# Kernel tuning notes

Measured on AMD Instinct MI355X. Metric: run time of the kernel, lower is better.

The kernel has to match this reference:

```python
import jax, jax.numpy as jnp
import numpy as np
from jax import lax

# ---- static config (from init_kwargs / input_specs) ----
B, NB, C, F = 16, 8192, 3, 64   # batches, points-per-batch, coord dim, feat dim
RATIO, K = 0.125, 16
M = int(RATIO * NB)


def setup_inputs() -> dict:
    key = jax.random.key(0)
    kx, kp = jax.random.split(key)
    x = jax.random.normal(kx, (B * NB, F), dtype=jnp.float32)
    pos = jax.random.normal(kp, (B * NB, C), dtype=jnp.float32)
    batch = (jnp.arange(B * NB, dtype=jnp.int32) // NB).astype(jnp.int32)
    return {"x": x, "pos": pos, "batch": batch}


def _fps_single(pos_b):
    """Sequential farthest point sampling on (NB, C), deterministic start at 0.
    Returns (M,) int32 indices into pos_b."""
    n = pos_b.shape[0]

    def step(carry, _):
        min_d2, last = carry
        d2 = jnp.sum((pos_b - pos_b[last]) ** 2, axis=-1)   # (NB,)
        min_d2 = jnp.minimum(min_d2, d2)
        nxt = jnp.argmax(min_d2).astype(jnp.int32)
        return (min_d2, nxt), last

    init = (jnp.full((n,), jnp.finfo(pos_b.dtype).max, dtype=pos_b.dtype),
            jnp.int32(0))
    _, idx = lax.scan(step, init, None, length=M)
    return idx  # (M,)


def reference(x, pos, batch):
    # batch ids are block-constant (batch[i] = i // NB), so per-batch views are
    # simple reshapes -- same semantics as torch_cluster's batched fps/knn.
    pos_b = pos.reshape(B, NB, C)

    # --- farthest point sampling per batch ---
    fps_idx = jax.vmap(_fps_single)(pos_b)                            # (B, M)
    centroids = jnp.take_along_axis(pos_b, fps_idx[..., None], axis=1)  # (B, M, C)

    # --- k-NN: squared distances centroids -> all points of same batch ---
    d2 = (jnp.sum(centroids ** 2, axis=-1)[..., None]
          - 2.0 * jnp.einsum('bmc,bnc->bmn', centroids, pos_b)
          + jnp.sum(pos_b ** 2, axis=-1)[:, None, :])                 # (B, M, NB)
    _, nn_idx = lax.top_k(-d2, K)                                     # (B, M, K)

    # gather neighbor coordinates (== pos[groups_idx[1]])
    groups = jax.vmap(lambda p, i: p[i])(pos_b, nn_idx.reshape(B, M * K))  # (B, M*K, C)

    return centroids.reshape(B * M, C), groups.reshape(B * M * K, C)
```

## Files before the change

kernel.cpp:

```cpp
#include <hip/hip_runtime.h>
#include <float.h>
#include <math.h>

#define B_   16
#define NB_  8192
#define M_   1024
#define K_   16


typedef float v2f __attribute__((ext_vector_type(2)));

#define FPS_T 256
#define PPT   32
#define NPAIR (PPT/2)
#define NWAVE (FPS_T/64)

__global__ __launch_bounds__(FPS_T, 1) void fps_kernel(const float* __restrict__ pos,
                                                       float* __restrict__ cent)
{
    #pragma clang fp contract(off)
    const int b = blockIdx.x;
    const int t = threadIdx.x;
    const float* pb = pos + (size_t)b * NB_ * 3;
    float* cb = cent + (size_t)b * M_ * 3;

    __shared__ float4 spts[NB_];
    __shared__ unsigned long long wkey[2][NWAVE];

    for (int p = t; p < NB_; p += FPS_T) {
        const float* s = pb + (size_t)p * 3;
        spts[p] = make_float4(s[0], s[1], s[2], 0.0f);
    }

    v2f px2[NPAIR], py2[NPAIR], pz2[NPAIR], md2[NPAIR];
    #pragma unroll
    for (int jj = 0; jj < NPAIR; ++jj) {
        const float* s0 = pb + (size_t)(t*PPT + 2*jj) * 3;
        px2[jj] = (v2f){s0[0], s0[3]};
        py2[jj] = (v2f){s0[1], s0[4]};
        pz2[jj] = (v2f){s0[2], s0[5]};
        md2[jj] = (v2f){FLT_MAX, FLT_MAX};
    }
    __syncthreads();

    float lx = pb[0], ly = pb[1], lz = pb[2];
    float c0x=0,c0y=0,c0z=0,c1x=0,c1y=0,c1z=0,c2x=0,c2y=0,c2z=0,c3x=0,c3y=0,c3z=0;

    for (int m = 0; m < M_; ++m) {
        if (t == (m >> 2)) {
            const int sl = m & 3;
            if      (sl == 0) { c0x=lx; c0y=ly; c0z=lz; }
            else if (sl == 1) { c1x=lx; c1y=ly; c1z=lz; }
            else if (sl == 2) { c2x=lx; c2y=ly; c2z=lz; }
            else              { c3x=lx; c3y=ly; c3z=lz; }
        }
        if (m == M_ - 1) break;

        const v2f lxv = {lx,lx}, lyv = {ly,ly}, lzv = {lz,lz};
        v2f bmax2 = {-1.0f, -1.0f};
        #pragma unroll
        for (int jj = 0; jj < NPAIR; ++jj) {
            v2f dx = px2[jj] - lxv;
            v2f dy = py2[jj] - lyv;
            v2f dz = pz2[jj] - lzv;
            v2f d2 = (dx*dx + dy*dy) + dz*dz;
            v2f mj = __builtin_elementwise_min(md2[jj], d2);
            md2[jj] = mj;
            bmax2 = __builtin_elementwise_max(bmax2, mj);
        }
        float bm = fmaxf(bmax2.x, bmax2.y);

        float v = bm;
        {
            int vi;
            vi = __builtin_amdgcn_update_dpp(__float_as_int(v), __float_as_int(v), 0xB1,  0xF, 0xF, false);
            v = fmaxf(v, __int_as_float(vi));
            vi = __builtin_amdgcn_update_dpp(__float_as_int(v), __float_as_int(v), 0x4E,  0xF, 0xF, false);
            v = fmaxf(v, __int_as_float(vi));
            vi = __builtin_amdgcn_update_dpp(__float_as_int(v), __float_as_int(v), 0x141, 0xF, 0xF, false);
            v = fmaxf(v, __int_as_float(vi));
            vi = __builtin_amdgcn_update_dpp(__float_as_int(v), __float_as_int(v), 0x140, 0xF, 0xF, false);
            v = fmaxf(v, __int_as_float(vi));
            vi = __builtin_amdgcn_update_dpp(__float_as_int(v), __float_as_int(v), 0x142, 0xF, 0xF, false);
            v = fmaxf(v, __int_as_float(vi));
            vi = __builtin_amdgcn_update_dpp(__float_as_int(v), __float_as_int(v), 0x143, 0xF, 0xF, false);
            v = fmaxf(v, __int_as_float(vi));
        }
        const float wv = __int_as_float(__builtin_amdgcn_readlane(__float_as_int(v), 63));

        int jp = -1;
        #pragma unroll
        for (int jj = NPAIR - 1; jj >= 0; --jj) {
            if (md2[jj].y == wv) jp = 2*jj + 1;
            if (md2[jj].x == wv) jp = 2*jj;
        }
        const unsigned long long mk = __ballot(jp >= 0);
        const int wl = (int)__ffsll(mk) - 1;
        const int gi = __builtin_amdgcn_readlane(t*PPT + jp, wl);

        const int par = m & 1;
        if ((t & 63) == 0)
            wkey[par][t >> 6] = ((unsigned long long)__float_as_uint(wv) << 32) |
                                (unsigned int)(~gi);
        __syncthreads();

        unsigned long long kk = wkey[par][0];
        #pragma unroll
        for (int w = 1; w < NWAVE; ++w) {
            const unsigned long long e = wkey[par][w];
            kk = (e > kk) ? e : kk;
        }
        const int best = (int)(~(unsigned int)kk);

        const float4 c = spts[best];
        lx = c.x; ly = c.y; lz = c.z;
    }

    {
        float4* o = (float4*)(cb + (size_t)t * 12);
        o[0] = make_float4(c0x, c0y, c0z, c1x);
        o[1] = make_float4(c1y, c1z, c2x, c2y);
        o[2] = make_float4(c2z, c3x, c3y, c3z);
    }
}

#define KNN_T   256
#define CHUNK   1024
#define GRP     8
#define BCAP    16
#define BSTRIDE 17

__device__ __forceinline__ void topk_insert(float d2, int pi, float val[16], int idx[16])
{
    int r = 0;
    #pragma unroll
    for (int j = 0; j < 16; ++j) r += (val[j] <= d2) ? 1 : 0;
    #pragma unroll
    for (int j = 15; j >= 1; --j) {
        bool sh = (j > r);
        val[j] = sh ? val[j-1] : val[j];
        idx[j] = sh ? idx[j-1] : idx[j];
    }
    #pragma unroll
    for (int j = 0; j < 16; ++j) {
        bool pl = (j == r);
        val[j] = pl ? d2 : val[j];
        idx[j] = pl ? pi : idx[j];
    }
}

__global__ __launch_bounds__(KNN_T, 2) void knn_kernel(const float* __restrict__ pos,
    const float* __restrict__ cent, float* __restrict__ groups,
    unsigned long long* __restrict__ partials, int nsplit)
{
    #pragma clang fp contract(off)
    __shared__ float4 spts[CHUNK];
    __shared__ unsigned long long sbuf[KNN_T * BSTRIDE];

    const int wg = blockIdx.x;
    const int t  = threadIdx.x;
    const int per_b = 4 * nsplit;
    const int b  = wg / per_b;
    const int r  = wg % per_b;
    const int cg = r / nsplit;
    const int sp = r % nsplit;
    const int span  = NB_ / nsplit;
    const int pbase = sp * span;
    const int nchunks = span / CHUNK;

    const float* pb = pos + (size_t)b * NB_ * 3;
    const int mg = b * M_ + cg * KNN_T + t;
    const float cx = cent[(size_t)mg*3+0];
    const float cy = cent[(size_t)mg*3+1];
    const float cz = cent[(size_t)mg*3+2];
    const float cn2 = (cx*cx + cy*cy) + cz*cz;

    float val[16]; int idx[16];
    #pragma unroll
    for (int j = 0; j < 16; ++j) { val[j] = FLT_MAX; idx[j] = 0; }
    float tau = FLT_MAX;
    int cnt = 0;
    unsigned long long* mybuf = sbuf + t * BSTRIDE;

    for (int c = 0; c < nchunks; ++c) {
        const int ps = pbase + c * CHUNK;
        __syncthreads();
        for (int p = t; p < CHUNK; p += KNN_T) {
            const float* s = pb + (size_t)(ps + p) * 3;
            float x = s[0], y = s[1], z = s[2];
            float pn2 = (x*x + y*y) + z*z;
            spts[p] = make_float4(x, y, z, pn2);
        }
        __syncthreads();

        for (int p0 = 0; p0 < CHUNK; p0 += GRP) {
            if (__any(cnt > BCAP - GRP)) {
                int n = cnt; cnt = 0;
                for (int i = 0; i < n; ++i) {
                    unsigned long long e = mybuf[i];
                    float d = __uint_as_float((unsigned int)(e >> 32));
                    int pi  = (int)(e & 0xFFFFFFFFu);
                    if (d < val[15]) topk_insert(d, pi, val, idx);
                }
                tau = val[15];
            }
            float4 q[GRP];
            #pragma unroll
            for (int i = 0; i < GRP; ++i) q[i] = spts[p0 + i];
            float d2v[GRP];
            #pragma unroll
            for (int i = 0; i < GRP; ++i) {
                float dot = __builtin_fmaf(cz, q[i].z,
                            __builtin_fmaf(cy, q[i].y, cx * q[i].x));
                d2v[i] = (cn2 - 2.0f*dot) + q[i].w;
            }
            #pragma unroll
            for (int i = 0; i < GRP; ++i) {
                if (d2v[i] < tau) {
                    mybuf[cnt] = ((unsigned long long)__float_as_uint(d2v[i]) << 32) |
                                 (unsigned int)(ps + p0 + i);
                    ++cnt;
                }
            }
        }
    }
    {
        int n = cnt;
        for (int i = 0; i < n; ++i) {
            unsigned long long e = mybuf[i];
            float d = __uint_as_float((unsigned int)(e >> 32));
            int pi  = (int)(e & 0xFFFFFFFFu);
            if (d < val[15]) topk_insert(d, pi, val, idx);
        }
    }

    if (nsplit > 1) {
        unsigned long long* o = partials + ((size_t)mg * nsplit + sp) * 16;
        #pragma unroll
        for (int kq = 0; kq < 16; ++kq)
            o[kq] = ((unsigned long long)__float_as_uint(val[kq]) << 32) | (unsigned int)idx[kq];
    } else {
        float* g = groups + (size_t)mg * K_ * 3;
        #pragma unroll
        for (int kq = 0; kq < 16; ++kq) {
            const float* s = pb + (size_t)idx[kq] * 3;
            g[kq*3+0] = s[0]; g[kq*3+1] = s[1]; g[kq*3+2] = s[2];
        }
    }
}

__global__ __launch_bounds__(256, 2) void knn_merge(const float* __restrict__ pos,
    const unsigned long long* __restrict__ partials, float* __restrict__ groups,
    int nsplit)
{
    const int mg = blockIdx.x * 256 + threadIdx.x;
    const int b  = mg >> 10;
    const float* pb = pos + (size_t)b * NB_ * 3;

    float val[16]; int idx[16];
    #pragma unroll
    for (int j = 0; j < 16; ++j) { val[j] = FLT_MAX; idx[j] = 0; }
    for (int sp = 0; sp < nsplit; ++sp) {
        const unsigned long long* l = partials + ((size_t)mg * nsplit + sp) * 16;
        #pragma unroll
        for (int kq = 0; kq < 16; ++kq) {
            unsigned long long e = l[kq];
            float d = __uint_as_float((unsigned int)(e >> 32));
            int pi  = (int)(e & 0xFFFFFFFFu);
            if (d < val[15]) topk_insert(d, pi, val, idx);
        }
    }
    float* g = groups + (size_t)mg * K_ * 3;
    #pragma unroll
    for (int kq = 0; kq < 16; ++kq) {
        const float* s = pb + (size_t)idx[kq] * 3;
        g[kq*3+0] = s[0]; g[kq*3+1] = s[1]; g[kq*3+2] = s[2];
    }
}

extern "C" void kernel_launch(void* const* d_in, const int* in_sizes, int n_in,
                              void* d_out, int out_size, void* d_ws, size_t ws_size,
                              hipStream_t stream)
{
    (void)in_sizes; (void)n_in; (void)out_size;
    const float* pos = (const float*)d_in[1];
    float* out    = (float*)d_out;
    float* cent   = out;
    float* groups = out + (size_t)B_ * M_ * 3;

    fps_kernel<<<B_, FPS_T, 0, stream>>>(pos, cent);

    const size_t lst = (size_t)B_ * M_ * 16 * sizeof(unsigned long long);
    int nsplit = (ws_size >= 8*lst) ? 8 : (ws_size >= 4*lst) ? 4 : (ws_size >= 2*lst) ? 2 : 1;

    knn_kernel<<<B_ * 4 * nsplit, KNN_T, 0, stream>>>(pos, cent, groups,
                                                      (unsigned long long*)d_ws, nsplit);
    if (nsplit > 1)
        knn_merge<<<(B_ * M_) / 256, 256, 0, stream>>>(pos,
                                                      (const unsigned long long*)d_ws,
                                                      groups, nsplit);
}
```

Measured before the change: 1.209 ms.

## Carry winner coords via registers in FPS; compress kNN partials to 16-bit indices

```diff
diff --git a/kernel.cpp b/kernel.cpp
--- a/kernel.cpp
+++ b/kernel.cpp
@@ -24,13 +24,8 @@
     const float* pb = pos + (size_t)b * NB_ * 3;
     float* cb = cent + (size_t)b * M_ * 3;
 
-    __shared__ float4 spts[NB_];
     __shared__ unsigned long long wkey[2][NWAVE];
-
-    for (int p = t; p < NB_; p += FPS_T) {
-        const float* s = pb + (size_t)p * 3;
-        spts[p] = make_float4(s[0], s[1], s[2], 0.0f);
-    }
+    __shared__ float4             wc[2][NWAVE];
 
     v2f px2[NPAIR], py2[NPAIR], pz2[NPAIR], md2[NPAIR];
     #pragma unroll
@@ -41,7 +36,6 @@
         pz2[jj] = (v2f){s0[2], s0[5]};
         md2[jj] = (v2f){FLT_MAX, FLT_MAX};
     }
-    __syncthreads();
 
     float lx = pb[0], ly = pb[1], lz = pb[2];
     float c0x=0,c0y=0,c0z=0,c1x=0,c1y=0,c1z=0,c2x=0,c2y=0,c2z=0,c3x=0,c3y=0,c3z=0;
@@ -98,22 +92,37 @@
         const int wl = (int)__ffsll(mk) - 1;
         const int gi = __builtin_amdgcn_readlane(t*PPT + jp, wl);
 
+        const int  pairi = jp >> 1;
+        const bool hihalf = (jp & 1) != 0;
+        float sxv = 0.f, syv = 0.f, szv = 0.f;
+        #pragma unroll
+        for (int jj = 0; jj < NPAIR; ++jj) {
+            const bool m2 = (pairi == jj);
+            const float hx = hihalf ? px2[jj].y : px2[jj].x;
+            const float hy = hihalf ? py2[jj].y : py2[jj].x;
+            const float hz = hihalf ? pz2[jj].y : pz2[jj].x;
+            sxv = m2 ? hx : sxv; syv = m2 ? hy : syv; szv = m2 ? hz : szv;
+        }
+        const float sxw = __int_as_float(__builtin_amdgcn_readlane(__float_as_int(sxv), wl));
+        const float syw = __int_as_float(__builtin_amdgcn_readlane(__float_as_int(syv), wl));
+        const float szw = __int_as_float(__builtin_amdgcn_readlane(__float_as_int(szv), wl));
+
         const int par = m & 1;
-        if ((t & 63) == 0)
-            wkey[par][t >> 6] = ((unsigned long long)__float_as_uint(wv) << 32) |
-                                (unsigned int)(~gi);
+        const int w   = t >> 6;
+        if ((t & 63) == 0) {
+            wkey[par][w] = ((unsigned long long)__float_as_uint(wv) << 32) |
+                           (unsigned int)(~gi);
+            wc[par][w]   = make_float4(sxw, syw, szw, 0.0f);
+        }
         __syncthreads();
 
-        unsigned long long kk = wkey[par][0];
-        #pragma unroll
-        for (int w = 1; w < NWAVE; ++w) {
-            const unsigned long long e = wkey[par][w];
-            kk = (e > kk) ? e : kk;
-        }
-        const int best = (int)(~(unsigned int)kk);
-
-        const float4 c = spts[best];
-        lx = c.x; ly = c.y; lz = c.z;
+        unsigned long long k0 = wkey[par][0], k1 = wkey[par][1],
+                           k2 = wkey[par][2], k3 = wkey[par][3];
+        float4 q0 = wc[par][0], q1 = wc[par][1], q2 = wc[par][2], q3 = wc[par][3];
+        if (k1 > k0) { k0 = k1; q0 = q1; }
+        if (k3 > k2) { k2 = k3; q2 = q3; }
+        if (k2 > k0) { k0 = k2; q0 = q2; }
+        lx = q0.x; ly = q0.y; lz = q0.z;
     }
 
     {
@@ -129,6 +138,7 @@
 #define GRP     8
 #define BCAP    16
 #define BSTRIDE 17
+#define NSPLIT  8
 
 __device__ __forceinline__ void topk_insert(float d2, int pi, float val[16], int idx[16])
 {
@@ -151,7 +161,7 @@
 
 __global__ __launch_bounds__(KNN_T, 2) void knn_kernel(const float* __restrict__ pos,
     const float* __restrict__ cent, float* __restrict__ groups,
-    unsigned long long* __restrict__ partials, int nsplit)
+    unsigned short* __restrict__ partials, int nsplit)
 {
     #pragma clang fp contract(off)
     __shared__ float4 spts[CHUNK];
@@ -235,10 +245,9 @@
     }
 
     if (nsplit > 1) {
-        unsigned long long* o = partials + ((size_t)mg * nsplit + sp) * 16;
-        #pragma unroll
-        for (int kq = 0; kq < 16; ++kq)
-            o[kq] = ((unsigned long long)__float_as_uint(val[kq]) << 32) | (unsigned int)idx[kq];
+        unsigned short* o = partials + ((size_t)mg * NSPLIT + sp) * 16;
+        #pragma unroll
+        for (int kq = 0; kq < 16; ++kq) o[kq] = (unsigned short)idx[kq];
     } else {
         float* g = groups + (size_t)mg * K_ * 3;
         #pragma unroll
@@ -249,25 +258,36 @@
     }
 }
 
-__global__ __launch_bounds__(256, 2) void knn_merge(const float* __restrict__ pos,
-    const unsigned long long* __restrict__ partials, float* __restrict__ groups,
-    int nsplit)
-{
-    const int mg = blockIdx.x * 256 + threadIdx.x;
+__global__ __launch_bounds__(64) void knn_merge(const float* __restrict__ pos,
+    const float* __restrict__ cent,
+    const unsigned short* __restrict__ partials, float* __restrict__ groups)
+{
+    #pragma clang fp contract(off)
+    const int mg = blockIdx.x * 64 + threadIdx.x;
     const int b  = mg >> 10;
     const float* pb = pos + (size_t)b * NB_ * 3;
 
+    const float cx = cent[(size_t)mg*3+0];
+    const float cy = cent[(size_t)mg*3+1];
+    const float cz = cent[(size_t)mg*3+2];
+    const float cn2 = (cx*cx + cy*cy) + cz*cz;
+
     float val[16]; int idx[16];
     #pragma unroll
     for (int j = 0; j < 16; ++j) { val[j] = FLT_MAX; idx[j] = 0; }
-    for (int sp = 0; sp < nsplit; ++sp) {
-        const unsigned long long* l = partials + ((size_t)mg * nsplit + sp) * 16;
+
+    for (int sp = 0; sp < NSPLIT; ++sp) {
+        const unsigned short* l = partials + ((size_t)mg * NSPLIT + sp) * 16;
         #pragma unroll
         for (int kq = 0; kq < 16; ++kq) {
-            unsigned long long e = l[kq];
-            float d = __uint_as_float((unsigned int)(e >> 32));
-            int pi  = (int)(e & 0xFFFFFFFFu);
-            if (d < val[15]) topk_insert(d, pi, val, idx);
+            const int pi = (int)l[kq];
+            const float* s = pb + (size_t)pi * 3;
+            const float x = s[0], y = s[1], z = s[2];
+            const float pn2 = (x*x + y*y) + z*z;
+            const float dot = __builtin_fmaf(cz, z,
+                              __builtin_fmaf(cy, y, cx * x));
+            const float d2  = (cn2 - 2.0f*dot) + pn2;
+            if (d2 < val[15]) topk_insert(d2, pi, val, idx);
         }
     }
     float* g = groups + (size_t)mg * K_ * 3;
@@ -290,13 +310,13 @@
 
     fps_kernel<<<B_, FPS_T, 0, stream>>>(pos, cent);
 
-    const size_t lst = (size_t)B_ * M_ * 16 * sizeof(unsigned long long);
-    int nsplit = (ws_size >= 8*lst) ? 8 : (ws_size >= 4*lst) ? 4 : (ws_size >= 2*lst) ? 2 : 1;
-
-    knn_kernel<<<B_ * 4 * nsplit, KNN_T, 0, stream>>>(pos, cent, groups,
-                                                      (unsigned long long*)d_ws, nsplit);
-    if (nsplit > 1)
-        knn_merge<<<(B_ * M_) / 256, 256, 0, stream>>>(pos,
-                                                      (const unsigned long long*)d_ws,
-                                                      groups, nsplit);
-}
+    const size_t need = (size_t)B_ * M_ * NSPLIT * 16 * sizeof(unsigned short);
+    if (ws_size >= need) {
+        knn_kernel<<<B_ * 4 * NSPLIT, KNN_T, 0, stream>>>(pos, cent, groups,
+                                                          (unsigned short*)d_ws, NSPLIT);
+        knn_merge<<<(B_ * M_) / 64, 64, 0, stream>>>(pos, cent,
+                                                     (const unsigned short*)d_ws, groups);
+    } else {
+        knn_kernel<<<B_ * 4, KNN_T, 0, stream>>>(pos, cent, groups, nullptr, 1);
+    }
+}
```

Measured after the change: 1.590 ms. 31.5% more time.
